# Optimization experiments

Hardware: AMD Instinct MI355X
Metric: run time of the kernel (lower is better)

The kernel has to match this reference:

```python
import jax, jax.numpy as jnp
import numpy as np

N, D = 8192, 1024
TEMPERATURE = 0.1
EPS = 1e-8

def setup_inputs() -> dict:
    key = jax.random.key(0)
    k1, k2 = jax.random.split(key)
    emb = jax.random.normal(k1, (N, D), dtype=jnp.float32)
    # docstring: embeddings are normalized
    emb = emb / jnp.linalg.norm(emb, axis=1, keepdims=True)
    labels = jax.random.randint(k2, (N,), 0, 2, dtype=jnp.int32)
    return {"embeddings": emb, "labels": labels}

def reference(embeddings, labels):
    lab = labels.astype(embeddings.dtype)            # (N,)
    sim = jnp.matmul(embeddings, embeddings.T) / TEMPERATURE  # (N, N)
    exp_sim = jnp.exp(sim)                           # original uses raw exp (no max-subtract)
    diag = jnp.diagonal(exp_sim)                     # self-similarity exp(1/T)
    # all_sim excludes self; pos_sim = other reference rows (labels==1, j != i)
    all_sum = exp_sim.sum(axis=1) - diag             # (N,)
    pos_sum = exp_sim @ lab - diag * lab             # subtract self only when i is ref
    loss_per_row = -jnp.log(pos_sum / (all_sum + EPS))
    n_ref = lab.sum()
    loss = jnp.sum(jnp.where(lab > 0, loss_per_row, 0.0)) / jnp.maximum(n_ref, 1.0)
    # original returns 0.0 when fewer than 2 reference rows
    return jnp.where(n_ref < 2, jnp.array(0.0, embeddings.dtype), loss)
```

## Files before the change

kernel.cpp:

```cpp
#include <hip/hip_runtime.h>
#include <hip/hip_bf16.h>
#include <cstdint>
#include <cstddef>

#define NROWS 8192
#define DIM   1024
#define BMR 256
#define BNC 128
#define BK  32
#define NKS (DIM / BK)
#define NBLK 1056
#define EPS 1e-8f
#define PRESCALE 3.798288f

#define ABUF 8192
#define BUFE 12288

typedef short  bf16x8  __attribute__((ext_vector_type(8)));
typedef float  floatx4 __attribute__((ext_vector_type(4)));

typedef __attribute__((address_space(1))) const void CGV;
typedef __attribute__((address_space(3))) void LV;

__device__ __forceinline__ void async_load16(const void* g, void* l) {
    __builtin_amdgcn_global_load_lds((CGV*)g, (LV*)l, 16, 0, 0);
}

__device__ __forceinline__ unsigned short f2bf_rne(float f) {
    union { float f; unsigned u; } c; c.f = f;
    unsigned u = c.u;
    unsigned r = (u + 0x7fffu + ((u >> 16) & 1u)) >> 16;
    return (unsigned short)r;
}

__global__ __launch_bounds__(256) void convert_kernel(
    const float* __restrict__ in, unsigned short* __restrict__ out,
    float* __restrict__ accum )
{
    int i = (blockIdx.x * 256 + threadIdx.x) * 4;
    float4 v = *(const float4*)(in + i);
    ushort4 o;
    o.x = f2bf_rne(v.x * PRESCALE);
    o.y = f2bf_rne(v.y * PRESCALE);
    o.z = f2bf_rne(v.z * PRESCALE);
    o.w = f2bf_rne(v.w * PRESCALE);
    *(ushort4*)(out + i) = o;
    if (blockIdx.x < (2 * NROWS) / 256)
        accum[blockIdx.x * 256 + threadIdx.x] = 0.0f;
}

__global__ __launch_bounds__(512, 4) void gemm_fused_kernel(
    const unsigned short* __restrict__ E,
    const int*            __restrict__ labels,
    float*                __restrict__ all_sum,
    float*                __restrict__ pos_sum)
{
    __shared__ __align__(16) unsigned short S[3 * BUFE];

    const int tid  = threadIdx.x;
    const int lane = tid & 63;
    const int w    = tid >> 6;
    const int wm   = w >> 1;
    const int wn   = w & 1;
    const int colw = lane & 15;
    const int quad = lane >> 4;

    const int b = blockIdx.x;
    const int t = (b & 7) * 132 + (b >> 3);
    int a = (int)((sqrtf(4.0f * (float)t + 1.0f) - 1.0f) * 0.5f);
    while ((a + 1) * (a + 2) <= t) ++a;
    while (a * (a + 1) > t) --a;
    const int c = t - a * (a + 1);

    const int rBase = a * BMR;
    const int cBase = c * BNC;

    const int l4  = lane >> 2;
    const int gch = (lane & 3) ^ (l4 & 3);
    const unsigned short* gA0 = E + (size_t)(rBase + w * 32 + l4) * DIM + gch * 8;
    const unsigned short* gA1 = gA0 + (size_t)16 * DIM;
    const unsigned short* gB  = E + (size_t)(cBase + w * 16 + l4) * DIM + gch * 8;
    const int aL0 = (w * 128 + lane) * 8;
    const int bL  = (w * 64 + lane) * 8;

    const int fs    = (quad ^ (colw & 3)) * 8;
    const int aBase = (wm * 64 + colw) * BK + fs;
    const int bBase = (wn * 64 + colw) * BK + fs;

    floatx4 acc[4][4];
    #pragma unroll
    for (int i = 0; i < 4; ++i)
        #pragma unroll
        for (int j = 0; j < 4; ++j)
            acc[i][j] = (floatx4)0.0f;

#define STAGE(T, SB) do { \
        async_load16(gA0 + (T) * BK, &S[(SB) * BUFE + aL0]);        \
        async_load16(gA1 + (T) * BK, &S[(SB) * BUFE + aL0 + 512]);  \
        async_load16(gB  + (T) * BK, &S[(SB) * BUFE + ABUF + bL]);  \
    } while (0)

    STAGE(0, 0);
    STAGE(1, 1);
    asm volatile("s_waitcnt vmcnt(3)" ::: "memory");
    __builtin_amdgcn_s_barrier();
    __builtin_amdgcn_sched_barrier(0);

    #pragma unroll
    for (int kt = 0; kt < NKS; ++kt) {
        const int rb = kt % 3;
        const int sb = (kt + 2) % 3;

        bf16x8 bF[4];
        #pragma unroll
        for (int nt = 0; nt < 4; ++nt)
            bF[nt] = *(const bf16x8*)&S[rb * BUFE + ABUF + bBase + nt * 16 * BK];

        if (kt < NKS - 2) STAGE(kt + 2, sb);

        __builtin_amdgcn_s_setprio(1);
        #pragma unroll
        for (int mt = 0; mt < 4; ++mt) {
            bf16x8 aF = *(const bf16x8*)&S[rb * BUFE + aBase + mt * 16 * BK];
            #pragma unroll
            for (int nt = 0; nt < 4; ++nt)
                acc[mt][nt] = __builtin_amdgcn_mfma_f32_16x16x32_bf16(
                    aF, bF[nt], acc[mt][nt], 0, 0, 0);
        }
        __builtin_amdgcn_s_setprio(0);

        __builtin_amdgcn_sched_barrier(0);
        if (kt < NKS - 2)
            asm volatile("s_waitcnt vmcnt(3) lgkmcnt(0)" ::: "memory");
        else
            asm volatile("s_waitcnt vmcnt(0) lgkmcnt(0)" ::: "memory");
        __builtin_amdgcn_s_barrier();
        __builtin_amdgcn_sched_barrier(0);
    }
#undef STAGE

    float labc[4];
    int   gcolv[4];
    #pragma unroll
    for (int nt = 0; nt < 4; ++nt) {
        gcolv[nt] = cBase + wn * 64 + nt * 16 + colw;
        labc[nt]  = (float)labels[gcolv[nt]];
    }

    float colAll[4] = {0.f, 0.f, 0.f, 0.f};
    float colPos[4] = {0.f, 0.f, 0.f, 0.f};

    #pragma unroll
    for (int mt = 0; mt < 4; ++mt) {
        const int growBase = rBase + wm * 64 + mt * 16 + quad * 4;
        #pragma unroll
        for (int r = 0; r < 4; ++r) {
            const int grow = growBase + r;
            const float labr = (float)labels[grow];
            float sAll = 0.f, sPos = 0.f;
            #pragma unroll
            for (int nt = 0; nt < 4; ++nt) {
                float ev = exp2f(acc[mt][nt][r]);
                ev = (grow > gcolv[nt]) ? ev : 0.0f;
                sAll += ev;
                sPos += ev * labc[nt];
                colAll[nt] += ev;
                colPos[nt] += ev * labr;
            }
            #pragma unroll
            for (int off = 1; off < 16; off <<= 1) {
                sAll += __shfl_xor(sAll, off);
                sPos += __shfl_xor(sPos, off);
            }
            if (colw == 0 && sAll != 0.f) {
                atomicAdd(&all_sum[grow], sAll);
                atomicAdd(&pos_sum[grow], sPos);
            }
        }
    }

    #pragma unroll
    for (int nt = 0; nt < 4; ++nt) {
        float aa = colAll[nt], p = colPos[nt];
        aa += __shfl_xor(aa, 16);  p += __shfl_xor(p, 16);
        aa += __shfl_xor(aa, 32);  p += __shfl_xor(p, 32);
        if (quad == 0 && aa != 0.f) {
            atomicAdd(&all_sum[gcolv[nt]], aa);
            atomicAdd(&pos_sum[gcolv[nt]], p);
        }
    }
}

__global__ __launch_bounds__(1024) void finalize_kernel(
    const float* __restrict__ all_sum,
    const float* __restrict__ pos_sum,
    const int*   __restrict__ labels,
    float*       __restrict__ out)
{
    __shared__ float sSum[1024];
    __shared__ float sCnt[1024];
    const int tid = threadIdx.x;
    float lsum = 0.f, lcnt = 0.f;
    for (int i = tid; i < NROWS; i += 1024) {
        if (labels[i] > 0) {
            float p = pos_sum[i];
            float a = all_sum[i] + EPS;
            lsum += -logf(p / a);
            lcnt += 1.0f;
        }
    }
    sSum[tid] = lsum;
    sCnt[tid] = lcnt;
    __syncthreads();
    for (int s = 512; s > 0; s >>= 1) {
        if (tid < s) { sSum[tid] += sSum[tid + s]; sCnt[tid] += sCnt[tid + s]; }
        __syncthreads();
    }
    if (tid == 0) {
        float n = sCnt[0];
        out[0] = (n < 2.0f) ? 0.0f : sSum[0] / fmaxf(n, 1.0f);
    }
}

extern "C" void kernel_launch(void* const* d_in, const int* in_sizes, int n_in,
                              void* d_out, int out_size, void* d_ws, size_t ws_size,
                              hipStream_t stream) {
    const float* emb    = (const float*)d_in[0];
    const int*   labels = (const int*)d_in[1];
    float*       out    = (float*)d_out;

    unsigned short* Ebf = (unsigned short*)d_ws;
    const size_t embBytes = (size_t)NROWS * DIM * sizeof(unsigned short);
    float* all_sum = (float*)((char*)d_ws + embBytes);
    float* pos_sum = all_sum + NROWS;

    convert_kernel<<<(NROWS * DIM) / (4 * 256), 256, 0, stream>>>(emb, Ebf, all_sum);

    gemm_fused_kernel<<<NBLK, 512, 0, stream>>>(Ebf, labels, all_sum, pos_sum);

    finalize_kernel<<<1, 1024, 0, stream>>>(all_sum, pos_sum, labels, out);
}
```

Baseline: 190.4 us.

## Use square 256x256 triangular tiles with diagonal-block MFMA skipping and BK=64

Replaces 256x128 tiles over the lower triangle with 256x256 square tiles: 496 full off-diagonal tiles plus 32 diagonal tiles, where waves skip MFMAs for sub-tiles entirely above the diagonal. Each wave now computes 128x64 outputs (8x4 accumulators), K step grows to 64 with double buffering and an 8-way XOR swizzle, and occupancy drops to 2 blocks per CU. The goal is higher arithmetic intensity and less redundant work above the diagonal, at the cost of more registers, more LDS and fewer resident waves for latency hiding. The wave-to-column mapping on diagonal tiles is permuted so the masked MFMA work is spread more evenly across waves.

After: 226.5 us. 1.19x slower.

```diff
diff --git a/kernel.cpp b/kernel.cpp
--- a/kernel.cpp
+++ b/kernel.cpp
@@ -5,16 +5,17 @@
 
 #define NROWS 8192
 #define DIM   1024
-#define BMR 256
-#define BNC 128
-#define BK  32
-#define NKS (DIM / BK)
-#define NBLK 1056
+#define BT    256
+#define BK    64
+#define NKT   (DIM / BK)
+#define NFULL 496
+#define NDIAG 32
+#define NBLK  (NFULL + NDIAG)
 #define EPS 1e-8f
 #define PRESCALE 3.798288f
 
-#define ABUF 8192
-#define BUFE 12288
+#define ABUF_E 16384
+#define BUF_E  32768
 
 typedef short  bf16x8  __attribute__((ext_vector_type(8)));
 typedef float  floatx4 __attribute__((ext_vector_type(4)));
@@ -49,94 +50,112 @@
         accum[blockIdx.x * 256 + threadIdx.x] = 0.0f;
 }
 
-__global__ __launch_bounds__(512, 4) void gemm_fused_kernel(
+__global__ __launch_bounds__(512, 2) void gemm_fused_kernel(
     const unsigned short* __restrict__ E,
     const int*            __restrict__ labels,
     float*                __restrict__ all_sum,
     float*                __restrict__ pos_sum)
 {
-    __shared__ __align__(16) unsigned short S[3 * BUFE];
+    __shared__ __align__(16) unsigned short S[2 * BUF_E];
 
     const int tid  = threadIdx.x;
     const int lane = tid & 63;
     const int w    = tid >> 6;
-    const int wm   = w >> 1;
-    const int wn   = w & 1;
+    const int wm   = (w < 4) ? 1 : 0;
+    const int wn   = (w < 4) ? w : ((0x0132 >> ((w & 3) * 4)) & 0xF);
     const int colw = lane & 15;
     const int quad = lane >> 4;
+    const int swz  = colw & 7;
 
     const int b = blockIdx.x;
-    const int t = (b & 7) * 132 + (b >> 3);
-    int a = (int)((sqrtf(4.0f * (float)t + 1.0f) - 1.0f) * 0.5f);
-    while ((a + 1) * (a + 2) <= t) ++a;
-    while (a * (a + 1) > t) --a;
-    const int c = t - a * (a + 1);
-
-    const int rBase = a * BMR;
-    const int cBase = c * BNC;
-
-    const int l4  = lane >> 2;
-    const int gch = (lane & 3) ^ (l4 & 3);
-    const unsigned short* gA0 = E + (size_t)(rBase + w * 32 + l4) * DIM + gch * 8;
-    const unsigned short* gA1 = gA0 + (size_t)16 * DIM;
-    const unsigned short* gB  = E + (size_t)(cBase + w * 16 + l4) * DIM + gch * 8;
-    const int aL0 = (w * 128 + lane) * 8;
-    const int bL  = (w * 64 + lane) * 8;
-
-    const int fs    = (quad ^ (colw & 3)) * 8;
-    const int aBase = (wm * 64 + colw) * BK + fs;
-    const int bBase = (wn * 64 + colw) * BK + fs;
-
-    floatx4 acc[4][4];
-    #pragma unroll
-    for (int i = 0; i < 4; ++i)
+    int rBase, cBase; bool isDiag;
+    if (b < NFULL) {
+        const int t = (b & 7) * 62 + (b >> 3);
+        int a = (int)((1.0f + sqrtf(1.0f + 8.0f * (float)t)) * 0.5f);
+        while (a * (a - 1) / 2 > t) --a;
+        while ((a + 1) * a / 2 <= t) ++a;
+        const int c = t - a * (a - 1) / 2;
+        rBase = a * BT; cBase = c * BT; isDiag = false;
+    } else {
+        const int p = b - NFULL;
+        rBase = p * BT; cBase = rBase; isDiag = true;
+    }
+
+    const int l8  = lane >> 3;
+    const int gch = (lane & 7) ^ l8;
+    const unsigned short* gA0 = E + (size_t)(rBase + w * 32 + l8) * DIM + gch * 8;
+    const unsigned short* gB0 = E + (size_t)(cBase + w * 32 + l8) * DIM + gch * 8;
+    const int aL = w * 2048 + lane * 8;
+
+    floatx4 acc[8][4];
+    #pragma unroll
+    for (int i = 0; i < 8; ++i)
         #pragma unroll
         for (int j = 0; j < 4; ++j)
             acc[i][j] = (floatx4)0.0f;
 
-#define STAGE(T, SB) do { \
-        async_load16(gA0 + (T) * BK, &S[(SB) * BUFE + aL0]);        \
-        async_load16(gA1 + (T) * BK, &S[(SB) * BUFE + aL0 + 512]);  \
-        async_load16(gB  + (T) * BK, &S[(SB) * BUFE + ABUF + bL]);  \
+#define STAGE(T, SB) do {                                                     \
+        const unsigned short* _ga = gA0 + (T) * BK;                           \
+        const unsigned short* _gb = gB0 + (T) * BK;                           \
+        unsigned short* _la = &S[(SB) * BUF_E + aL];                          \
+        unsigned short* _lb = &S[(SB) * BUF_E + ABUF_E + aL];                 \
+        _Pragma("unroll")                                                     \
+        for (int j = 0; j < 4; ++j) {                                         \
+            async_load16(_ga + j * (8 * DIM), _la + j * 512);                 \
+            async_load16(_gb + j * (8 * DIM), _lb + j * 512);                 \
+        }                                                                     \
     } while (0)
+
+#define KLOOP(MASKCHECK)                                                      \
+    for (int kt = 0; kt < NKT; ++kt) {                                        \
+        const int bb = (kt & 1) * BUF_E;                                      \
+        _Pragma("unroll")                                                     \
+        for (int ksub = 0; ksub < 2; ++ksub) {                                \
+            const int cs = (((ksub << 2) | quad) ^ swz) << 3;                 \
+            bf16x8 bF[4], aF[8];                                              \
+            _Pragma("unroll")                                                 \
+            for (int nt = 0; nt < 4; ++nt)                                    \
+                bF[nt] = *(const bf16x8*)&S[bb + ABUF_E +                     \
+                              (wn * 64 + nt * 16 + colw) * BK + cs];          \
+            _Pragma("unroll")                                                 \
+            for (int mt = 0; mt < 8; ++mt)                                    \
+                aF[mt] = *(const bf16x8*)&S[bb +                              \
+                              (wm * 128 + mt * 16 + colw) * BK + cs];         \
+            __builtin_amdgcn_s_setprio(1);                                    \
+            _Pragma("unroll")                                                 \
+            for (int mt = 0; mt < 8; ++mt)                                    \
+                _Pragma("unroll")                                             \
+                for (int nt = 0; nt < 4; ++nt)                                \
+                    if (MASKCHECK)                                            \
+                        acc[mt][nt] = __builtin_amdgcn_mfma_f32_16x16x32_bf16(\
+                            aF[mt], bF[nt], acc[mt][nt], 0, 0, 0);            \
+            __builtin_amdgcn_s_setprio(0);                                    \
+        }                                                                     \
+        __builtin_amdgcn_sched_barrier(0);                                    \
+        __builtin_amdgcn_s_barrier();            \
+        __builtin_amdgcn_sched_barrier(0);                                    \
+        if (kt < NKT - 2) {                                                   \
+            STAGE(kt + 2, kt & 1);                                            \
+            asm volatile("s_waitcnt vmcnt(8)" ::: "memory");                  \
+        } else {                                                              \
+            asm volatile("s_waitcnt vmcnt(0)" ::: "memory");                  \
+        }                                                                     \
+        __builtin_amdgcn_s_barrier();                \
+        __builtin_amdgcn_sched_barrier(0);                                    \
+    }
 
     STAGE(0, 0);
     STAGE(1, 1);
-    asm volatile("s_waitcnt vmcnt(3)" ::: "memory");
+    asm volatile("s_waitcnt vmcnt(8)" ::: "memory");
     __builtin_amdgcn_s_barrier();
     __builtin_amdgcn_sched_barrier(0);
 
-    #pragma unroll
-    for (int kt = 0; kt < NKS; ++kt) {
-        const int rb = kt % 3;
-        const int sb = (kt + 2) % 3;
-
-        bf16x8 bF[4];
-        #pragma unroll
-        for (int nt = 0; nt < 4; ++nt)
-            bF[nt] = *(const bf16x8*)&S[rb * BUFE + ABUF + bBase + nt * 16 * BK];
-
-        if (kt < NKS - 2) STAGE(kt + 2, sb);
-
-        __builtin_amdgcn_s_setprio(1);
-        #pragma unroll
-        for (int mt = 0; mt < 4; ++mt) {
-            bf16x8 aF = *(const bf16x8*)&S[rb * BUFE + aBase + mt * 16 * BK];
-            #pragma unroll
-            for (int nt = 0; nt < 4; ++nt)
-                acc[mt][nt] = __builtin_amdgcn_mfma_f32_16x16x32_bf16(
-                    aF, bF[nt], acc[mt][nt], 0, 0, 0);
-        }
-        __builtin_amdgcn_s_setprio(0);
-
-        __builtin_amdgcn_sched_barrier(0);
-        if (kt < NKS - 2)
-            asm volatile("s_waitcnt vmcnt(3) lgkmcnt(0)" ::: "memory");
-        else
-            asm volatile("s_waitcnt vmcnt(0) lgkmcnt(0)" ::: "memory");
-        __builtin_amdgcn_s_barrier();
-        __builtin_amdgcn_sched_barrier(0);
-    }
+    if (!isDiag) {
+        KLOOP(true)
+    } else {
+        KLOOP(wm * 128 + mt * 16 + 15 >= wn * 64 + nt * 16)
+    }
+#undef KLOOP
 #undef STAGE
 
     float labc[4];
@@ -151,8 +170,8 @@
     float colPos[4] = {0.f, 0.f, 0.f, 0.f};
 
     #pragma unroll
-    for (int mt = 0; mt < 4; ++mt) {
-        const int growBase = rBase + wm * 64 + mt * 16 + quad * 4;
+    for (int mt = 0; mt < 8; ++mt) {
+        const int growBase = rBase + wm * 128 + mt * 16 + quad * 4;
         #pragma unroll
         for (int r = 0; r < 4; ++r) {
             const int grow = growBase + r;
```

## Switch to square 128x128 triangular tiles with BK=64 and double buffering

Applied to the files above, without the earlier changes.

Replaces the 256x128 tile, 8-wave, triple-buffered GEMM with a 128x128 tile computed by 4 waves. Each k-step now covers 64 elements and uses an 8-way XOR LDS swizzle, with a simple double buffer synchronised by __syncthreads instead of hand-tuned waitcnt and barrier. Square tiles make the lower-triangle block mapping cleaner and waste less work on diagonal blocks. In exchange, the smaller tile lowers data reuse per load, and the coarser synchronisation may expose load latency that the previous pipeline hid.

Measured after the change: 244.6 us. 1.28x slower.

```diff
diff --git a/kernel.cpp b/kernel.cpp
--- a/kernel.cpp
+++ b/kernel.cpp
@@ -5,16 +5,16 @@
 
 #define NROWS 8192
 #define DIM   1024
-#define BMR 256
+#define BMR 128
 #define BNC 128
-#define BK  32
-#define NKS (DIM / BK)
-#define NBLK 1056
+#define BK  64
+#define NKT (DIM / BK)
+#define NBLK 2080
 #define EPS 1e-8f
 #define PRESCALE 3.798288f
 
-#define ABUF 8192
-#define BUFE 12288
+#define ABUF_E 8192
+#define BUF_E  16384
 
 typedef short  bf16x8  __attribute__((ext_vector_type(8)));
 typedef float  floatx4 __attribute__((ext_vector_type(4)));
@@ -49,13 +49,13 @@
         accum[blockIdx.x * 256 + threadIdx.x] = 0.0f;
 }
 
-__global__ __launch_bounds__(512, 4) void gemm_fused_kernel(
+__global__ __launch_bounds__(256, 2) void gemm_fused_kernel(
     const unsigned short* __restrict__ E,
     const int*            __restrict__ labels,
     float*                __restrict__ all_sum,
     float*                __restrict__ pos_sum)
 {
-    __shared__ __align__(16) unsigned short S[3 * BUFE];
+    __shared__ __align__(16) unsigned short S[2 * BUF_E];
 
     const int tid  = threadIdx.x;
     const int lane = tid & 63;
@@ -64,28 +64,36 @@
     const int wn   = w & 1;
     const int colw = lane & 15;
     const int quad = lane >> 4;
+    const int swz  = colw & 7;
+    const int cs0  = ((0 | quad) ^ swz) << 3;
+    const int cs1  = ((4 | quad) ^ swz) << 3;
 
     const int b = blockIdx.x;
-    const int t = (b & 7) * 132 + (b >> 3);
-    int a = (int)((sqrtf(4.0f * (float)t + 1.0f) - 1.0f) * 0.5f);
-    while ((a + 1) * (a + 2) <= t) ++a;
-    while (a * (a + 1) > t) --a;
-    const int c = t - a * (a + 1);
-
-    const int rBase = a * BMR;
-    const int cBase = c * BNC;
-
-    const int l4  = lane >> 2;
-    const int gch = (lane & 3) ^ (l4 & 3);
-    const unsigned short* gA0 = E + (size_t)(rBase + w * 32 + l4) * DIM + gch * 8;
-    const unsigned short* gA1 = gA0 + (size_t)16 * DIM;
-    const unsigned short* gB  = E + (size_t)(cBase + w * 16 + l4) * DIM + gch * 8;
-    const int aL0 = (w * 128 + lane) * 8;
-    const int bL  = (w * 64 + lane) * 8;
-
-    const int fs    = (quad ^ (colw & 3)) * 8;
-    const int aBase = (wm * 64 + colw) * BK + fs;
-    const int bBase = (wn * 64 + colw) * BK + fs;
+    const int t = (b & 7) * 260 + (b >> 3);
+    int bi = (int)((sqrtf(8.0f * (float)t + 1.0f) - 1.0f) * 0.5f);
+    while ((bi + 1) * (bi + 2) / 2 <= t) ++bi;
+    while (bi * (bi + 1) / 2 > t) --bi;
+    const int bj = t - bi * (bi + 1) / 2;
+
+    const int rBase = bi * BMR;
+    const int cBase = bj * BNC;
+
+    const int l8  = lane >> 3;
+    const int gch = (lane & 7) ^ l8;
+    const unsigned short* gA = E + (size_t)(rBase + w * 8 + l8) * DIM + gch * 8;
+    const unsigned short* gB = E + (size_t)(cBase + w * 8 + l8) * DIM + gch * 8;
+    const int ldsT = w * 512 + lane * 8;
+
+#define STAGE(T, SB) do {                                                     \
+        const size_t _gk = (size_t)(T) * BK;                                  \
+        _Pragma("unroll")                                                     \
+        for (int j = 0; j < 4; ++j) {                                         \
+            async_load16(gA + (size_t)j * (32 * DIM) + _gk,                   \
+                         &S[(SB) * BUF_E + j * 2048 + ldsT]);                 \
+            async_load16(gB + (size_t)j * (32 * DIM) + _gk,                   \
+                         &S[(SB) * BUF_E + ABUF_E + j * 2048 + ldsT]);        \
+        }                                                                     \
+    } while (0)
 
     floatx4 acc[4][4];
     #pragma unroll
@@ -94,48 +102,35 @@
         for (int j = 0; j < 4; ++j)
             acc[i][j] = (floatx4)0.0f;
 
-#define STAGE(T, SB) do { \
-        async_load16(gA0 + (T) * BK, &S[(SB) * BUFE + aL0]);        \
-        async_load16(gA1 + (T) * BK, &S[(SB) * BUFE + aL0 + 512]);  \
-        async_load16(gB  + (T) * BK, &S[(SB) * BUFE + ABUF + bL]);  \
-    } while (0)
-
     STAGE(0, 0);
-    STAGE(1, 1);
-    asm volatile("s_waitcnt vmcnt(3)" ::: "memory");
-    __builtin_amdgcn_s_barrier();
-    __builtin_amdgcn_sched_barrier(0);
-
-    #pragma unroll
-    for (int kt = 0; kt < NKS; ++kt) {
-        const int rb = kt % 3;
-        const int sb = (kt + 2) % 3;
-
-        bf16x8 bF[4];
+    __syncthreads();
+
+    for (int kt = 0; kt < NKT; ++kt) {
+        if (kt < NKT - 1) STAGE(kt + 1, (kt + 1) & 1);
+
+        const int bb = (kt & 1) * BUF_E;
+
         #pragma unroll
-        for (int nt = 0; nt < 4; ++nt)
-            bF[nt] = *(const bf16x8*)&S[rb * BUFE + ABUF + bBase + nt * 16 * BK];
-
-        if (kt < NKS - 2) STAGE(kt + 2, sb);
-
-        __builtin_amdgcn_s_setprio(1);
-        #pragma unroll
-        for (int mt = 0; mt < 4; ++mt) {
-            bf16x8 aF = *(const bf16x8*)&S[rb * BUFE + aBase + mt * 16 * BK];
+        for (int ksub = 0; ksub < 2; ++ksub) {
+            const int cs = ksub ? cs1 : cs0;
+            bf16x8 aF[4], bF[4];
             #pragma unroll
             for (int nt = 0; nt < 4; ++nt)
-                acc[mt][nt] = __builtin_amdgcn_mfma_f32_16x16x32_bf16(
-                    aF, bF[nt], acc[mt][nt], 0, 0, 0);
-        }
-        __builtin_amdgcn_s_setprio(0);
-
-        __builtin_amdgcn_sched_barrier(0);
-        if (kt < NKS - 2)
-            asm volatile("s_waitcnt vmcnt(3) lgkmcnt(0)" ::: "memory");
-        else
-            asm volatile("s_waitcnt vmcnt(0) lgkmcnt(0)" ::: "memory");
-        __builtin_amdgcn_s_barrier();
-        __builtin_amdgcn_sched_barrier(0);
+                bF[nt] = *(const bf16x8*)&S[bb + ABUF_E +
+                              (wn * 64 + nt * 16 + colw) * BK + cs];
+            #pragma unroll
+            for (int mt = 0; mt < 4; ++mt)
+                aF[mt] = *(const bf16x8*)&S[bb +
+                              (wm * 64 + mt * 16 + colw) * BK + cs];
+            #pragma unroll
+            for (int mt = 0; mt < 4; ++mt)
+                #pragma unroll
+                for (int nt = 0; nt < 4; ++nt)
+                    acc[mt][nt] = __builtin_amdgcn_mfma_f32_16x16x32_bf16(
+                        aF[mt], bF[nt], acc[mt][nt], 0, 0, 0);
+        }
+
+        __syncthreads();
     }
 #undef STAGE
 
@@ -236,7 +231,7 @@
 
     convert_kernel<<<(NROWS * DIM) / (4 * 256), 256, 0, stream>>>(emb, Ebf, all_sum);
 
-    gemm_fused_kernel<<<NBLK, 512, 0, stream>>>(Ebf, labels, all_sum, pos_sum);
+    gemm_fused_kernel<<<NBLK, 256, 0, stream>>>(Ebf, labels, all_sum, pos_sum);
 
     finalize_kernel<<<1, 1024, 0, stream>>>(all_sum, pos_sum, labels, out);
 }
```
